# Performance work log

Measured on AMD Instinct MI355X. Metric: run time of the kernel, lower is better.

The kernel has to match this reference:

```python
import math
import jax, jax.numpy as jnp
import numpy as np

NUM_HEADS = 12
HEAD_DIM = 64
HIDDEN = NUM_HEADS * HEAD_DIM  # 768
SEQ = 4096


def setup_inputs() -> dict:
    key = jax.random.key(0)
    ks = jax.random.split(key, 7)
    s = 0.02  # BERT-style init scale for weights
    return {
        "hidden_states": jax.random.normal(ks[0], (1, SEQ, HIDDEN), jnp.float32),
        "Wq": jax.random.normal(ks[1], (HIDDEN, HIDDEN), jnp.float32) * s,
        "bq": jax.random.normal(ks[2], (HIDDEN,), jnp.float32) * s,
        "Wk": jax.random.normal(ks[3], (HIDDEN, HIDDEN), jnp.float32) * s,
        "bk": jax.random.normal(ks[4], (HIDDEN,), jnp.float32) * s,
        "Wv": jax.random.normal(ks[5], (HIDDEN, HIDDEN), jnp.float32) * s,
        "bv": jax.random.normal(ks[6], (HIDDEN,), jnp.float32) * s,
    }


def _split_heads(z):
    # [S, HIDDEN] -> [H, S, dh]
    S = z.shape[0]
    return jnp.transpose(z.reshape(S, NUM_HEADS, HEAD_DIM), (1, 0, 2))


def reference(hidden_states, Wq, bq, Wk, bk, Wv, bv):
    # batch is squeezed in the original module (kernel is unbatched)
    x = hidden_states[0]  # [S, D]
    q = _split_heads(x @ Wq.T + bq)  # [H, S, dh]
    k = _split_heads(x @ Wk.T + bk)  # [H, S, dh]
    scale = 1.0 / math.sqrt(HEAD_DIM)
    scores = jnp.einsum('hqd,hkd->hqk', q, k) * scale  # [H, S, S]
    probs = jax.nn.softmax(scores, axis=-1)
    # multi_rand_attn_cuda approximates P @ (x @ Wv^T + bv) via CDF-driven
    # Monte-Carlo column sampling of Wv; its expectation is the exact product,
    # which is the correctness baseline computed here.
    v = _split_heads(x @ Wv.T + bv)  # [H, S, dh]
    ctx = jnp.einsum('hqk,hkd->hqd', probs, v)  # [H, S, dh]
    ctx = jnp.transpose(ctx, (1, 0, 2)).reshape(x.shape[0], HIDDEN)
    return ctx[None]  # [1, S, D]
```

## Files before the change

kernel.cpp:

```cpp
#include <hip/hip_runtime.h>
#include <stdint.h>


typedef float    f32x4 __attribute__((ext_vector_type(4)));
typedef _Float16 h16x8 __attribute__((ext_vector_type(8)));
typedef _Float16 h16x4 __attribute__((ext_vector_type(4)));
typedef _Float16 h16x2 __attribute__((ext_vector_type(2)));
typedef __fp16   fp16x2 __attribute__((ext_vector_type(2)));
typedef unsigned short u16;

#define MFMA32(A, B, C) __builtin_amdgcn_mfma_f32_16x16x32_f16((A), (B), (C), 0, 0, 0)
#define ZERO4 ((f32x4){0.f, 0.f, 0.f, 0.f})

#define SEQ 4096
#define HID 768
#define NH  12
#define DH  64

#define CEXP 0.18033688011112042f

#define WAITV(N) asm volatile("s_waitcnt vmcnt(" #N ")" ::: "memory")

__device__ __forceinline__ u16 f2h(float f) {
  union { _Float16 h; u16 u; } v;
  v.h = (_Float16)f;
  return v.u;
}
__device__ __forceinline__ float h2f(u16 u) {
  union { u16 u; _Float16 h; } v;
  v.u = u;
  return (float)v.h;
}

__device__ __forceinline__ void gload_lds16(const void* g, void* l) {
  __builtin_amdgcn_global_load_lds(
      (__attribute__((address_space(1))) void*)(g),
      (__attribute__((address_space(3))) void*)(l),
      16, 0, 0);
}

__global__ __launch_bounds__(256) void cast_all_k(
    const float* __restrict__ x,  const float* __restrict__ wq,
    const float* __restrict__ wk, const float* __restrict__ wv,
    u16* __restrict__ xh,  u16* __restrict__ wqh,
    u16* __restrict__ wkh, u16* __restrict__ wvh)
{
  int i = blockIdx.x * 256 + threadIdx.x;
  const int NX4 = (SEQ * HID) / 4;
  const int NW4 = (HID * HID) / 4;
  const float4* src; ushort4* dst; int idx;
  if (i < NX4) {
    src = (const float4*)x; dst = (ushort4*)xh; idx = i;
  } else {
    int j = i - NX4;
    int w = j / NW4;
    idx = j - w * NW4;
    src = (const float4*)(w == 0 ? wq : (w == 1 ? wk : wv));
    dst = (ushort4*)(w == 0 ? wqh : (w == 1 ? wkh : wvh));
  }
  float4 v = src[idx];
  ushort4 o;
  o.x = f2h(v.x); o.y = f2h(v.y); o.z = f2h(v.z); o.w = f2h(v.w);
  dst[idx] = o;
}

__global__ __launch_bounds__(256, 3) void qkv_gemm_k(
    const u16* __restrict__ xh,
    const u16* __restrict__ wqh, const u16* __restrict__ wkh, const u16* __restrict__ wvh,
    const float* __restrict__ bq, const float* __restrict__ bk, const float* __restrict__ bv,
    u16* __restrict__ Qh, u16* __restrict__ Kh, u16* __restrict__ Vt)
{
  __shared__ u16 S[128 * 128];

  const int t = threadIdx.x;
  const int wave = t >> 6, lane = t & 63;
  const int m = lane & 15, quad = lane >> 4;
  const int z  = blockIdx.z;
  const int n0 = blockIdx.x * 128;
  const int m0 = blockIdx.y * 128;

  const u16*   W    = (z == 0) ? wqh : (z == 1) ? wkh : wvh;
  const float* bias = (z == 0) ? bq  : (z == 1) ? bk  : bv;

  const int wm = (wave >> 1) * 64;
  const int wn = (wave & 1) * 64;

  f32x4 acc[4][4];
#pragma unroll
  for (int i = 0; i < 4; i++)
#pragma unroll
    for (int j = 0; j < 4; j++) acc[i][j] = ZERO4;

  const int srow = wave * 8 + (lane >> 3);
  const int scg  = (lane & 7) ^ (srow & 7);
  const u16* gA = xh + (m0 + srow) * HID + scg * 8;
  const u16* gB = W  + (n0 + srow) * HID + scg * 8;
  u16* lA = S + wave * 512;
  u16* lB = S + 8192 + wave * 512;

  for (int k0 = 0; k0 < HID; k0 += 64) {
    __syncthreads();
#pragma unroll
    for (int c = 0; c < 4; c++) {
      gload_lds16(gA + c * 32 * HID + k0, lA + c * 2048);
      gload_lds16(gB + c * 32 * HID + k0, lB + c * 2048);
    }
    __syncthreads();

#pragma unroll
    for (int s = 0; s < 2; s++) {
      h16x8 af[4], bf[4];
#pragma unroll
      for (int i = 0; i < 4; i++)
        af[i] = *(const h16x8*)(S + (wm + i * 16 + m) * 64
                                + ((s * 4 + quad) ^ (m & 7)) * 8);
#pragma unroll
      for (int j = 0; j < 4; j++)
        bf[j] = *(const h16x8*)(S + 8192 + (wn + j * 16 + m) * 64
                                + ((s * 4 + quad) ^ (m & 7)) * 8);
#pragma unroll
      for (int i = 0; i < 4; i++)
#pragma unroll
        for (int j = 0; j < 4; j++)
          acc[i][j] = MFMA32(af[i], bf[j], acc[i][j]);
    }
  }

  __syncthreads();

  if (z < 2) {
    const float sc = (z == 0) ? CEXP : 1.0f;
#pragma unroll
    for (int i = 0; i < 4; i++) {
      int sl = wm + i * 16 + quad * 4;
#pragma unroll
      for (int j = 0; j < 4; j++) {
        int colp = wn + j * 16 + m;
        float bb = bias[n0 + colp];
        int c = colp >> 3, sub = colp & 7;
#pragma unroll
        for (int r = 0; r < 4; r++)
          S[(sl + r) * 128 + ((c ^ ((sl + r) & 15)) * 8) + sub] =
              f2h((acc[i][j][r] + bb) * sc);
      }
    }
    __syncthreads();
    u16* outp = (z == 0) ? Qh : Kh;
    const int ch = t & 15;
#pragma unroll
    for (int rr = 0; rr < 8; rr++) {
      int s = rr * 16 + (t >> 4);
      h16x8 v = *(const h16x8*)(S + s * 128 + ((ch ^ (s & 15)) * 8));
      *(h16x8*)(outp + (m0 + s) * HID + n0 + ch * 8) = v;
    }
  } else {
#pragma unroll
    for (int i = 0; i < 4; i++) {
      int sl = wm + i * 16 + quad * 4;
      int vp = (sl & ~31) + ((sl >> 2) & 3) * 8 + ((sl >> 4) & 1) * 4;
#pragma unroll
      for (int j = 0; j < 4; j++) {
        int nl = wn + j * 16 + m;
        float bb = bias[n0 + nl];
        h16x4 o;
        o[0] = (_Float16)(acc[i][j][0] + bb);
        o[1] = (_Float16)(acc[i][j][1] + bb);
        o[2] = (_Float16)(acc[i][j][2] + bb);
        o[3] = (_Float16)(acc[i][j][3] + bb);
        *(h16x4*)(S + nl * 128 + (((vp >> 3) ^ (nl & 15)) * 8) + (vp & 7)) = o;
      }
    }
    __syncthreads();
    const int ch = t & 15;
#pragma unroll
    for (int rr = 0; rr < 8; rr++) {
      int n = rr * 16 + (t >> 4);
      h16x8 v = *(const h16x8*)(S + n * 128 + ((ch ^ (n & 15)) * 8));
      *(h16x8*)(Vt + (n0 + n) * SEQ + m0 + ch * 8) = v;
    }
  }
}


__device__ __forceinline__ void stage_kv(const u16* gKb, const u16* gVb,
                                         u16* lK, u16* lV, int kv0)
{
#pragma unroll
  for (int c = 0; c < 2; c++) {
    gload_lds16(gKb + (kv0 + c * 32) * HID, lK + c * 2048);
    gload_lds16(gVb + c * 32 * SEQ + kv0,   lV + c * 2048);
  }
}

__device__ __forceinline__ void attn_compute(
    const u16* __restrict__ Kb, const u16* __restrict__ Vb,
    const h16x8 (&qf)[2][2], f32x4 (&O)[2][4], f32x4 (&Lacc)[2],
    h16x8 onesv, int m, int quad)
{
#pragma unroll
  for (int p = 0; p < 2; ++p) {
    const int krow0 = 32 * p + m;
    const int krow1 = krow0 + 16;
    h16x8 kb00 = *(const h16x8*)(Kb + krow0 * 64 + ((    quad) ^ (m & 7)) * 8);
    h16x8 kb01 = *(const h16x8*)(Kb + krow0 * 64 + ((4 + quad) ^ (m & 7)) * 8);
    h16x8 kb10 = *(const h16x8*)(Kb + krow1 * 64 + ((    quad) ^ (m & 7)) * 8);
    h16x8 kb11 = *(const h16x8*)(Kb + krow1 * 64 + ((4 + quad) ^ (m & 7)) * 8);

    h16x8 vb[4];
#pragma unroll
    for (int jd = 0; jd < 4; jd++) {
      int d = jd * 16 + m;
      vb[jd] = *(const h16x8*)(Vb + d * 64 + (((p * 4 + quad) ^ (m & 7)) * 8));
    }

#pragma unroll
    for (int qn = 0; qn < 2; qn++) {
      __builtin_amdgcn_s_setprio(1);
      f32x4 S0 = MFMA32(kb00, qf[qn][0], ZERO4);
      S0       = MFMA32(kb01, qf[qn][1], S0);
      f32x4 S1 = MFMA32(kb10, qf[qn][0], ZERO4);
      S1       = MFMA32(kb11, qf[qn][1], S1);
      __builtin_amdgcn_s_setprio(0);

      float e0 = __builtin_amdgcn_exp2f(S0[0]);
      float e1 = __builtin_amdgcn_exp2f(S0[1]);
      float e2 = __builtin_amdgcn_exp2f(S0[2]);
      float e3 = __builtin_amdgcn_exp2f(S0[3]);
      float e4 = __builtin_amdgcn_exp2f(S1[0]);
      float e5 = __builtin_amdgcn_exp2f(S1[1]);
      float e6 = __builtin_amdgcn_exp2f(S1[2]);
      float e7 = __builtin_amdgcn_exp2f(S1[3]);

      fp16x2 p01 = __builtin_amdgcn_cvt_pkrtz(e0, e1);
      fp16x2 p23 = __builtin_amdgcn_cvt_pkrtz(e2, e3);
      fp16x2 p45 = __builtin_amdgcn_cvt_pkrtz(e4, e5);
      fp16x2 p67 = __builtin_amdgcn_cvt_pkrtz(e6, e7);
      h16x2 q01 = __builtin_bit_cast(h16x2, p01);
      h16x2 q23 = __builtin_bit_cast(h16x2, p23);
      h16x2 q45 = __builtin_bit_cast(h16x2, p45);
      h16x2 q67 = __builtin_bit_cast(h16x2, p67);
      h16x4 pl = __builtin_shufflevector(q01, q23, 0, 1, 2, 3);
      h16x4 ph = __builtin_shufflevector(q45, q67, 0, 1, 2, 3);
      h16x8 pa = __builtin_shufflevector(pl, ph, 0, 1, 2, 3, 4, 5, 6, 7);

      __builtin_amdgcn_s_setprio(1);
#pragma unroll
      for (int jd = 0; jd < 4; jd++)
        O[qn][jd] = MFMA32(pa, vb[jd], O[qn][jd]);
      Lacc[qn] = MFMA32(pa, onesv, Lacc[qn]);
      __builtin_amdgcn_s_setprio(0);
    }
  }
}

__global__ __launch_bounds__(256, 3) void attn_k(
    const u16* __restrict__ Qh, const u16* __restrict__ Kh, const u16* __restrict__ Vt,
    float* __restrict__ out0, u16* __restrict__ Op1, float* __restrict__ Lp)
{
  __shared__ u16 Ks[2][64 * 64];
  __shared__ u16 Vs[2][64 * 64];

  const int t = threadIdx.x;
  const int wave = t >> 6, lane = t & 63;
  const int m = lane & 15, quad = lane >> 4;
  const int h  = blockIdx.y;
  const int q0 = blockIdx.x * 128;
  const int sp = blockIdx.z;
  const int kvbase = sp * 2048;

  h16x8 qf[2][2];
#pragma unroll
  for (int qn = 0; qn < 2; qn++)
#pragma unroll
    for (int ks = 0; ks < 2; ks++)
      qf[qn][ks] = *(const h16x8*)(Qh + (q0 + wave * 32 + qn * 16 + m) * HID
                                   + h * DH + ks * 32 + quad * 8);

  f32x4 O[2][4];
#pragma unroll
  for (int qn = 0; qn < 2; qn++)
#pragma unroll
    for (int jd = 0; jd < 4; jd++) O[qn][jd] = ZERO4;
  f32x4 Lacc[2] = {ZERO4, ZERO4};

  h16x8 onesv;
#pragma unroll
  for (int j = 0; j < 8; j++) onesv[j] = (_Float16)1.0f;

  const int srow = wave * 8 + (lane >> 3);
  const int swz  = ((lane & 7) ^ (srow & 7)) * 8;
  const u16* gKb = Kh + srow * HID + h * DH + swz;
  const u16* gVb = Vt + (h * DH + srow) * SEQ + swz;
  u16* lK0 = &Ks[0][wave * 512];
  u16* lK1 = &Ks[1][wave * 512];
  u16* lV0 = &Vs[0][wave * 512];
  u16* lV1 = &Vs[1][wave * 512];

  stage_kv(gKb, gVb, lK0, lV0, kvbase);

  for (int it = 0; it < 32; it += 2) {
    stage_kv(gKb, gVb, lK1, lV1, kvbase + (it + 1) * 64);
    WAITV(4);
    __builtin_amdgcn_s_barrier();
    __builtin_amdgcn_sched_barrier(0);
    attn_compute(&Ks[0][0], &Vs[0][0], qf, O, Lacc, onesv, m, quad);
    __builtin_amdgcn_s_barrier();
    __builtin_amdgcn_sched_barrier(0);

    if (it + 2 < 32) {
      stage_kv(gKb, gVb, lK0, lV0, kvbase + (it + 2) * 64);
      WAITV(4);
    } else {
      WAITV(0);
    }
    __builtin_amdgcn_s_barrier();
    __builtin_amdgcn_sched_barrier(0);
    attn_compute(&Ks[1][0], &Vs[1][0], qf, O, Lacc, onesv, m, quad);
    __builtin_amdgcn_s_barrier();
    __builtin_amdgcn_sched_barrier(0);
  }

#pragma unroll
  for (int qn = 0; qn < 2; qn++) {
    if (m == 0) {
#pragma unroll
      for (int r = 0; r < 4; r++)
        Lp[sp * NH * SEQ + h * SEQ + q0 + wave * 32 + qn * 16 + quad * 4 + r] =
            Lacc[qn][r];
    }
#pragma unroll
    for (int jd = 0; jd < 4; jd++) {
      int col = h * DH + jd * 16 + m;
#pragma unroll
      for (int r = 0; r < 4; r++) {
        int row = q0 + wave * 32 + qn * 16 + quad * 4 + r;
        if (sp == 0) out0[row * HID + col] = O[qn][jd][r];
        else         Op1[row * HID + col] = f2h(O[qn][jd][r]);
      }
    }
  }
}

__global__ __launch_bounds__(256) void reduce_k(
    float* __restrict__ out, const u16* __restrict__ Op1,
    const float* __restrict__ Lp)
{
  int i = blockIdx.x * 256 + threadIdx.x;
  int s  = i / 192;
  int c4 = i - s * 192;
  int h  = c4 >> 4;
  float L = Lp[h * SEQ + s] + Lp[NH * SEQ + h * SEQ + s];
  float inv = __builtin_amdgcn_rcpf(L);
  float4 a = ((const float4*)out)[i];
  ushort4 b = ((const ushort4*)Op1)[i];
  float4 r;
  r.x = (a.x + h2f(b.x)) * inv;
  r.y = (a.y + h2f(b.y)) * inv;
  r.z = (a.z + h2f(b.z)) * inv;
  r.w = (a.w + h2f(b.w)) * inv;
  ((float4*)out)[i] = r;
}

extern "C" void kernel_launch(void* const* d_in, const int* in_sizes, int n_in,
                              void* d_out, int out_size, void* d_ws, size_t ws_size,
                              hipStream_t stream) {
  const float* x  = (const float*)d_in[0];
  const float* Wq = (const float*)d_in[1];
  const float* bq = (const float*)d_in[2];
  const float* Wk = (const float*)d_in[3];
  const float* bk = (const float*)d_in[4];
  const float* Wv = (const float*)d_in[5];
  const float* bv = (const float*)d_in[6];
  float* out = (float*)d_out;

  char* ws = (char*)d_ws;
  u16* Qh  = (u16*)(ws);
  u16* Kh  = (u16*)(ws + 6291456);
  u16* Vt  = (u16*)(ws + 12582912);
  u16* xh  = (u16*)(ws + 18874368);
  u16* wqh = (u16*)(ws + 25165824);
  u16* wkh = (u16*)(ws + 26345472);
  u16* wvh = (u16*)(ws + 27525120);
  u16*   Op1 = (u16*)(ws + 18874368);
  float* Lp  = (float*)(ws + 25165824);

  cast_all_k<<<4800, 256, 0, stream>>>(x, Wq, Wk, Wv, xh, wqh, wkh, wvh);
  qkv_gemm_k<<<dim3(6, 32, 3), 256, 0, stream>>>(xh, wqh, wkh, wvh,
                                                 bq, bk, bv, Qh, Kh, Vt);
  attn_k<<<dim3(32, NH, 2), 256, 0, stream>>>(Qh, Kh, Vt, out, Op1, Lp);
  reduce_k<<<3072, 256, 0, stream>>>(out, Op1, Lp);
}
```

Measured before the change: 159.2 us.

## Triple-buffer K/V tiles in LDS to keep two loads in flight

Switches the attention kernel's K/V staging from double to triple buffering. Each iteration now needs only one barrier instead of two, and the next-next tile's load is issued right after the barrier so global loads overlap more compute. The cost is 50% more LDS per block (48KB), which may limit occupancy at the 3-blocks-per-CU launch bound.

```diff
diff --git a/kernel.cpp b/kernel.cpp
--- a/kernel.cpp
+++ b/kernel.cpp
@@ -20,6 +20,8 @@
 #define CEXP 0.18033688011112042f
 
 #define WAITV(N) asm volatile("s_waitcnt vmcnt(" #N ")" ::: "memory")
+#define SBAR()   __builtin_amdgcn_s_barrier()
+#define SCHED0() __builtin_amdgcn_sched_barrier(0)
 
 __device__ __forceinline__ u16 f2h(float f) {
   union { _Float16 h; u16 u; } v;
@@ -257,8 +259,8 @@
     const u16* __restrict__ Qh, const u16* __restrict__ Kh, const u16* __restrict__ Vt,
     float* __restrict__ out0, u16* __restrict__ Op1, float* __restrict__ Lp)
 {
-  __shared__ u16 Ks[2][64 * 64];
-  __shared__ u16 Vs[2][64 * 64];
+  __shared__ u16 Ks[3][64 * 64];
+  __shared__ u16 Vs[3][64 * 64];
 
   const int t = threadIdx.x;
   const int wave = t >> 6, lane = t & 63;
@@ -291,34 +293,34 @@
   const int swz  = ((lane & 7) ^ (srow & 7)) * 8;
   const u16* gKb = Kh + srow * HID + h * DH + swz;
   const u16* gVb = Vt + (h * DH + srow) * SEQ + swz;
-  u16* lK0 = &Ks[0][wave * 512];
-  u16* lK1 = &Ks[1][wave * 512];
-  u16* lV0 = &Vs[0][wave * 512];
-  u16* lV1 = &Vs[1][wave * 512];
+  u16* lK0 = &Ks[0][wave * 512]; u16* lV0 = &Vs[0][wave * 512];
+  u16* lK1 = &Ks[1][wave * 512]; u16* lV1 = &Vs[1][wave * 512];
+  u16* lK2 = &Ks[2][wave * 512]; u16* lV2 = &Vs[2][wave * 512];
 
   stage_kv(gKb, gVb, lK0, lV0, kvbase);
-
-  for (int it = 0; it < 32; it += 2) {
-    stage_kv(gKb, gVb, lK1, lV1, kvbase + (it + 1) * 64);
-    WAITV(4);
-    __builtin_amdgcn_s_barrier();
-    __builtin_amdgcn_sched_barrier(0);
+  stage_kv(gKb, gVb, lK1, lV1, kvbase + 64);
+
+  for (int it = 0; it < 30; it += 3) {
+    WAITV(4); SBAR(); SCHED0();
+    stage_kv(gKb, gVb, lK2, lV2, kvbase + (it + 2) * 64);
     attn_compute(&Ks[0][0], &Vs[0][0], qf, O, Lacc, onesv, m, quad);
-    __builtin_amdgcn_s_barrier();
-    __builtin_amdgcn_sched_barrier(0);
-
-    if (it + 2 < 32) {
-      stage_kv(gKb, gVb, lK0, lV0, kvbase + (it + 2) * 64);
-      WAITV(4);
-    } else {
-      WAITV(0);
-    }
-    __builtin_amdgcn_s_barrier();
-    __builtin_amdgcn_sched_barrier(0);
+    SCHED0();
+
+    WAITV(4); SBAR(); SCHED0();
+    stage_kv(gKb, gVb, lK0, lV0, kvbase + (it + 3) * 64);
     attn_compute(&Ks[1][0], &Vs[1][0], qf, O, Lacc, onesv, m, quad);
-    __builtin_amdgcn_s_barrier();
-    __builtin_amdgcn_sched_barrier(0);
-  }
+    SCHED0();
+
+    WAITV(4); SBAR(); SCHED0();
+    stage_kv(gKb, gVb, lK1, lV1, kvbase + (it + 4) * 64);
+    attn_compute(&Ks[2][0], &Vs[2][0], qf, O, Lacc, onesv, m, quad);
+    SCHED0();
+  }
+  WAITV(4); SBAR(); SCHED0();
+  attn_compute(&Ks[0][0], &Vs[0][0], qf, O, Lacc, onesv, m, quad);
+  SCHED0();
+  WAITV(0); SBAR(); SCHED0();
+  attn_compute(&Ks[1][0], &Vs[1][0], qf, O, Lacc, onesv, m, quad);
 
 #pragma unroll
   for (int qn = 0; qn < 2; qn++) {
```

After: 158.1 us. About the same (-0.7%).
